# Kernel optimization log

Measured on AMD Instinct MI355X. Metric: run time of the kernel, lower is better.

## Reference

```python
import jax, jax.numpy as jnp
import numpy as np

B, D, H = 262144, 3, 64


def _mlp(params, x):
    # x: [D] -> scalar u
    (W1, b1), (W2, b2), (W3, b3), (W4, b4) = params
    h = jnp.tanh(x @ W1 + b1)
    h = jnp.tanh(h @ W2 + b2)
    h = jnp.tanh(h @ W3 + b3)
    return (h @ W4 + b4)[0]


def setup_inputs() -> dict:
    key = jax.random.key(0)
    ks = jax.random.split(key, 6)
    def glorot(k, shape):
        fan_in = shape[0]
        return jax.random.normal(k, shape, dtype=jnp.float32) / jnp.sqrt(jnp.float32(fan_in))
    return {
        "x_r": jax.random.normal(ks[0], (B, D), dtype=jnp.float32),
        "sigma_r": jax.random.uniform(ks[1], (B,), dtype=jnp.float32),
        "W1": glorot(ks[2], (D, H)), "b1": jnp.zeros((H,), jnp.float32),
        "W2": glorot(ks[3], (H, H)), "b2": jnp.zeros((H,), jnp.float32),
        "W3": glorot(ks[4], (H, H)), "b3": jnp.zeros((H,), jnp.float32),
        "W4": glorot(ks[5], (H, 1)), "b4": jnp.zeros((1,), jnp.float32),
    }


def reference(x_r, sigma_r, W1, b1, W2, b2, W3, b3, W4, b4):
    # r(x) = div( sigma * grad u(x) ) = trace( d(flux)/dx ), per sample.
    params = ((W1, b1), (W2, b2), (W3, b3), (W4, b4))

    def flux_single(x, s):
        # sigma * grad_u, shape [D]
        return s * jax.grad(lambda xx: _mlp(params, xx))(x)

    def div_single(x, s):
        # forward-over-reverse: jacfwd of reverse-mode grad -> [D, D]; take trace
        J = jax.jacfwd(lambda xx: flux_single(xx, s))(x)
        return jnp.trace(J)

    div = jax.vmap(div_single)(x_r, sigma_r)  # [B]
    return div[:, None]
```

## Files before the change

kernel.cpp:

```cpp
#include <hip/hip_runtime.h>

typedef __fp16 f16;
typedef f16  h8 __attribute__((ext_vector_type(8)));
typedef float f4 __attribute__((ext_vector_type(4)));
typedef unsigned u32t;

#define NBLOCKS 1024
#define WPB 4
#define SPW 64
#define NBATCH 4
#define XSTR 36
#define XST  (16 * XSTR)

union H8u { h8 v; u32t u[4]; };
union U4h { uint4 u; h8 v; };

__device__ __forceinline__ u32t pk2(float a, float b) {
    return __builtin_bit_cast(u32t, __builtin_amdgcn_cvt_pkrtz(a, b));
}

__device__ __forceinline__ void tanh_sech2(float a, float& h, float& g) {
    float E = __expf(2.f * a);
    float inv = __builtin_amdgcn_rcpf(E + 1.f);
    float u = inv + inv;
    h = 1.f - u;
    g = u * (2.f - u);
}

__global__ __launch_bounds__(256, 3) void pinn_mfma_kernel(
    const float* __restrict__ x_r, const float* __restrict__ sigma_r,
    const float* __restrict__ W1, const float* __restrict__ b1,
    const float* __restrict__ W2, const float* __restrict__ b2,
    const float* __restrict__ W3, const float* __restrict__ b3,
    const float* __restrict__ W4, float* __restrict__ out)
{
    __shared__ f4 Wg[64];
    __shared__ f4 Wb4[16], B2v[16], B3v[16], W4v[16];
    __shared__ u32t xch[WPB][5 * XST];

    const int tid = threadIdx.x, lane = tid & 63, wv = tid >> 6;
    const int sb = lane & 15;
    const int q  = lane >> 4;

    if (tid < 64) {
        float wx = W1[tid], wy = W1[64 + tid], wz = W1[128 + tid];
        f4 w; w[0] = wx; w[1] = wy; w[2] = wz;
        w[3] = -2.f * (wx * wx + wy * wy + wz * wz);
        Wg[tid] = w;
        ((float*)Wb4)[tid] = b1[tid];
        ((float*)B2v)[tid] = b2[tid];
        ((float*)B3v)[tid] = b3[tid];
        ((float*)W4v)[tid] = W4[tid];
    }
    __syncthreads();

    h8 A2f[4][2], A3f[4][2];
#pragma unroll
    for (int mt = 0; mt < 4; ++mt)
#pragma unroll
    for (int kk = 0; kk < 2; ++kk) {
        H8u t2, t3;
#pragma unroll
        for (int p = 0; p < 4; ++p) {
            const int r0 = (32 * kk + 8 * q + 2 * p) * 64 + 16 * mt + sb;
            t2.u[p] = pk2(W2[r0], W2[r0 + 64]);
            t3.u[p] = pk2(W3[r0], W3[r0 + 64]);
        }
        A2f[mt][kk] = t2.v; A3f[mt][kk] = t3.v;
    }

    u32t* xb = xch[wv];
    const int wbase = sb * XSTR + 2 * q;
    const int rbase = sb * XSTR + 4 * q;

    const long sbase = ((long)blockIdx.x * WPB + wv) * SPW;

    float nx0 = x_r[(sbase + sb) * 3], nx1 = x_r[(sbase + sb) * 3 + 1],
          nx2 = x_r[(sbase + sb) * 3 + 2], nsg = sigma_r[sbase + sb];

#define WR5(mt) { const int wo = wbase + 8 * (mt);                                         \
    *(uint2*)&xb[0 * XST + wo] = make_uint2(pk2(oh[0], oh[1]), pk2(oh[2], oh[3]));         \
    *(uint2*)&xb[1 * XST + wo] = make_uint2(pk2(ox[0], ox[1]), pk2(ox[2], ox[3]));         \
    *(uint2*)&xb[2 * XST + wo] = make_uint2(pk2(oy[0], oy[1]), pk2(oy[2], oy[3]));         \
    *(uint2*)&xb[3 * XST + wo] = make_uint2(pk2(oz[0], oz[1]), pk2(oz[2], oz[3]));         \
    *(uint2*)&xb[4 * XST + wo] = make_uint2(pk2(os[0], os[1]), pk2(os[2], os[3])); }

#define RDB(Bf, st) { U4h u0, u1;                                                          \
    u0.u = *(const uint4*)&xb[(st) * XST + rbase];                                         \
    u1.u = *(const uint4*)&xb[(st) * XST + rbase + 16];                                    \
    Bf[0] = u0.v; Bf[1] = u1.v; }

#define MFMA10(Af) _Pragma("unroll")                                                       \
    for (int kk = 0; kk < 2; ++kk) {                                                       \
        Ch = __builtin_amdgcn_mfma_f32_16x16x32_f16(Af[mt][kk], Bh[kk], Ch, 0, 0, 0);      \
        Cx = __builtin_amdgcn_mfma_f32_16x16x32_f16(Af[mt][kk], Bx[kk], Cx, 0, 0, 0);      \
        Cy = __builtin_amdgcn_mfma_f32_16x16x32_f16(Af[mt][kk], By[kk], Cy, 0, 0, 0);      \
        Cz = __builtin_amdgcn_mfma_f32_16x16x32_f16(Af[mt][kk], Bz[kk], Cz, 0, 0, 0);      \
        Cs = __builtin_amdgcn_mfma_f32_16x16x32_f16(Af[mt][kk], Bs[kk], Cs, 0, 0, 0);      \
    }

#pragma unroll 1
    for (int t = 0; t < NBATCH; ++t) {
        const float x0 = nx0, x1 = nx1, x2 = nx2, sg = nsg;
        const long sn = sbase + ((t + 1) & 3) * 16 + sb;
        nx0 = x_r[sn * 3]; nx1 = x_r[sn * 3 + 1]; nx2 = x_r[sn * 3 + 2];
        nsg = sigma_r[sn];

#pragma unroll
        for (int mt = 0; mt < 4; ++mt) {
            const f4 bb = Wb4[4 * mt + q];
            float oh[4], ox[4], oy[4], oz[4], os[4];
#pragma unroll
            for (int r = 0; r < 4; ++r) {
                const f4 w = Wg[16 * mt + 4 * q + r];
                float a = fmaf(w[0], x0, fmaf(w[1], x1, fmaf(w[2], x2, bb[r])));
                float h, g; tanh_sech2(a, h, g);
                oh[r] = h; ox[r] = g * w[0]; oy[r] = g * w[1]; oz[r] = g * w[2];
                os[r] = (h * g) * w[3];
            }
            WR5(mt)
        }

        h8 Bh[2], Bx[2], By[2], Bz[2], Bs[2];
        RDB(Bh, 0) RDB(Bx, 1) RDB(By, 2) RDB(Bz, 3) RDB(Bs, 4)

#pragma unroll
        for (int mt = 0; mt < 4; ++mt) {
            f4 Ch = {0.f,0.f,0.f,0.f}, Cx = {0.f,0.f,0.f,0.f}, Cy = {0.f,0.f,0.f,0.f},
               Cz = {0.f,0.f,0.f,0.f}, Cs = {0.f,0.f,0.f,0.f};
            MFMA10(A2f)
            const f4 bb = B2v[4 * mt + q];
            float oh[4], ox[4], oy[4], oz[4], os[4];
#pragma unroll
            for (int r = 0; r < 4; ++r) {
                float h, g; tanh_sech2(Ch[r] + bb[r], h, g);
                float ax = Cx[r], ay = Cy[r], az = Cz[r];
                float qq  = fmaf(ax, ax, fmaf(ay, ay, az * az));
                float hg2 = (h * g) * 2.f;
                oh[r] = h; ox[r] = g * ax; oy[r] = g * ay; oz[r] = g * az;
                os[r] = fmaf(g, Cs[r], -(hg2 * qq));
            }
            WR5(mt)
        }

        RDB(Bh, 0) RDB(Bx, 1) RDB(By, 2) RDB(Bz, 3) RDB(Bs, 4)

        float tot = 0.f;
#pragma unroll
        for (int mt = 0; mt < 4; ++mt) {
            f4 Ch = {0.f,0.f,0.f,0.f}, Cx = {0.f,0.f,0.f,0.f}, Cy = {0.f,0.f,0.f,0.f},
               Cz = {0.f,0.f,0.f,0.f}, Cs = {0.f,0.f,0.f,0.f};
            MFMA10(A3f)
            const f4 bb = B3v[4 * mt + q], w4 = W4v[4 * mt + q];
#pragma unroll
            for (int r = 0; r < 4; ++r) {
                float h, g; tanh_sech2(Ch[r] + bb[r], h, g);
                float ax = Cx[r], ay = Cy[r], az = Cz[r];
                float qq  = fmaf(ax, ax, fmaf(ay, ay, az * az));
                float hg2 = (h * g) * 2.f;
                float sv  = fmaf(g, Cs[r], -(hg2 * qq));
                tot = fmaf(sv, w4[r], tot);
            }
        }
        tot += __shfl_xor(tot, 16);
        tot += __shfl_xor(tot, 32);
        if (lane < 16) out[sbase + t * 16 + sb] = sg * tot;
    }
}

extern "C" void kernel_launch(void* const* d_in, const int* in_sizes, int n_in,
                              void* d_out, int out_size, void* d_ws, size_t ws_size,
                              hipStream_t stream) {
    const float* x_r     = (const float*)d_in[0];
    const float* sigma_r = (const float*)d_in[1];
    const float* W1      = (const float*)d_in[2];
    const float* b1      = (const float*)d_in[3];
    const float* W2      = (const float*)d_in[4];
    const float* b2      = (const float*)d_in[5];
    const float* W3      = (const float*)d_in[6];
    const float* b3      = (const float*)d_in[7];
    const float* W4      = (const float*)d_in[8];
    float* out = (float*)d_out;

    pinn_mfma_kernel<<<NBLOCKS, 256, 0, stream>>>(
        x_r, sigma_r, W1, b1, W2, b2, W3, b3, W4, out);
}
```

Measured before the change: 44.14 us.

## Use grid-stride batch loop with fewer blocks and fold 2/ln2 into tanh bias

Each wave no longer owns a fixed run of four 16-sample batches. Instead, 768 blocks walk batches with a grid-stride loop, and the next batch's x/sigma loads are prefetched. The tanh argument now goes straight to exp2, with the 2*log2(e) factor folded into precomputed biases and an FMA, which removes a multiply per activation. With fewer blocks, waves do an uneven number of batches, so load balance depends on how 768 blocks map onto the CUs.

```diff
diff --git a/kernel.cpp b/kernel.cpp
--- a/kernel.cpp
+++ b/kernel.cpp
@@ -5,12 +5,13 @@
 typedef float f4 __attribute__((ext_vector_type(4)));
 typedef unsigned u32t;
 
-#define NBLOCKS 1024
+#define NBLOCKS 768
 #define WPB 4
-#define SPW 64
-#define NBATCH 4
+#define NWAVES (NBLOCKS * WPB)
+#define NBAT (262144 / 16)
 #define XSTR 36
 #define XST  (16 * XSTR)
+#define K2L 2.8853900817779268f
 
 union H8u { h8 v; u32t u[4]; };
 union U4h { uint4 u; h8 v; };
@@ -19,8 +20,8 @@
     return __builtin_bit_cast(u32t, __builtin_amdgcn_cvt_pkrtz(a, b));
 }
 
-__device__ __forceinline__ void tanh_sech2(float a, float& h, float& g) {
-    float E = __expf(2.f * a);
+__device__ __forceinline__ void tanh_sech2_t(float t, float& h, float& g) {
+    float E = __builtin_amdgcn_exp2f(t);
     float inv = __builtin_amdgcn_rcpf(E + 1.f);
     float u = inv + inv;
     h = 1.f - u;
@@ -35,7 +36,7 @@
     const float* __restrict__ W4, float* __restrict__ out)
 {
     __shared__ f4 Wg[64];
-    __shared__ f4 Wb4[16], B2v[16], B3v[16], W4v[16];
+    __shared__ f4 Wb4[16], BbK2[16], BbK3[16], W4v[16];
     __shared__ u32t xch[WPB][5 * XST];
 
     const int tid = threadIdx.x, lane = tid & 63, wv = tid >> 6;
@@ -47,10 +48,10 @@
         f4 w; w[0] = wx; w[1] = wy; w[2] = wz;
         w[3] = -2.f * (wx * wx + wy * wy + wz * wz);
         Wg[tid] = w;
-        ((float*)Wb4)[tid] = b1[tid];
-        ((float*)B2v)[tid] = b2[tid];
-        ((float*)B3v)[tid] = b3[tid];
-        ((float*)W4v)[tid] = W4[tid];
+        ((float*)Wb4)[tid]  = b1[tid];
+        ((float*)BbK2)[tid] = K2L * b2[tid];
+        ((float*)BbK3)[tid] = K2L * b3[tid];
+        ((float*)W4v)[tid]  = W4[tid];
     }
     __syncthreads();
 
@@ -73,10 +74,7 @@
     const int wbase = sb * XSTR + 2 * q;
     const int rbase = sb * XSTR + 4 * q;
 
-    const long sbase = ((long)blockIdx.x * WPB + wv) * SPW;
-
-    float nx0 = x_r[(sbase + sb) * 3], nx1 = x_r[(sbase + sb) * 3 + 1],
-          nx2 = x_r[(sbase + sb) * 3 + 2], nsg = sigma_r[sbase + sb];
+    const int wave_global = blockIdx.x * WPB + wv;
 
 #define WR5(mt) { const int wo = wbase + 8 * (mt);                                         \
     *(uint2*)&xb[0 * XST + wo] = make_uint2(pk2(oh[0], oh[1]), pk2(oh[2], oh[3]));         \
@@ -99,10 +97,20 @@
         Cs = __builtin_amdgcn_mfma_f32_16x16x32_f16(Af[mt][kk], Bs[kk], Cs, 0, 0, 0);      \
     }
 
+    int b = wave_global;
+    {
+        const long sp = (long)b * 16 + sb;
+    }
+    long sp0 = (long)b * 16 + sb;
+    float nx0 = x_r[sp0 * 3], nx1 = x_r[sp0 * 3 + 1], nx2 = x_r[sp0 * 3 + 2],
+          nsg = sigma_r[sp0];
+
 #pragma unroll 1
-    for (int t = 0; t < NBATCH; ++t) {
+    for (; b < NBAT; b += NWAVES) {
         const float x0 = nx0, x1 = nx1, x2 = nx2, sg = nsg;
-        const long sn = sbase + ((t + 1) & 3) * 16 + sb;
+        int bn = b + NWAVES;
+        if (bn >= NBAT) bn = wave_global;
+        const long sn = (long)bn * 16 + sb;
         nx0 = x_r[sn * 3]; nx1 = x_r[sn * 3 + 1]; nx2 = x_r[sn * 3 + 2];
         nsg = sigma_r[sn];
 
@@ -113,8 +121,8 @@
 #pragma unroll
             for (int r = 0; r < 4; ++r) {
                 const f4 w = Wg[16 * mt + 4 * q + r];
-                float a = fmaf(w[0], x0, fmaf(w[1], x1, fmaf(w[2], x2, bb[r])));
-                float h, g; tanh_sech2(a, h, g);
+                const float a = fmaf(w[0], x0, fmaf(w[1], x1, fmaf(w[2], x2, bb[r])));
+                float h, g; tanh_sech2_t(K2L * a, h, g);
                 oh[r] = h; ox[r] = g * w[0]; oy[r] = g * w[1]; oz[r] = g * w[2];
                 os[r] = (h * g) * w[3];
             }
@@ -129,14 +137,14 @@
             f4 Ch = {0.f,0.f,0.f,0.f}, Cx = {0.f,0.f,0.f,0.f}, Cy = {0.f,0.f,0.f,0.f},
                Cz = {0.f,0.f,0.f,0.f}, Cs = {0.f,0.f,0.f,0.f};
             MFMA10(A2f)
-            const f4 bb = B2v[4 * mt + q];
+            const f4 bb = BbK2[4 * mt + q];
             float oh[4], ox[4], oy[4], oz[4], os[4];
 #pragma unroll
             for (int r = 0; r < 4; ++r) {
-                float h, g; tanh_sech2(Ch[r] + bb[r], h, g);
-                float ax = Cx[r], ay = Cy[r], az = Cz[r];
-                float qq  = fmaf(ax, ax, fmaf(ay, ay, az * az));
-                float hg2 = (h * g) * 2.f;
+                float h, g; tanh_sech2_t(fmaf(Ch[r], K2L, bb[r]), h, g);
+                const float ax = Cx[r], ay = Cy[r], az = Cz[r];
+                const float qq  = fmaf(ax, ax, fmaf(ay, ay, az * az));
+                const float hg2 = (h * g) * 2.f;
                 oh[r] = h; ox[r] = g * ax; oy[r] = g * ay; oz[r] = g * az;
                 os[r] = fmaf(g, Cs[r], -(hg2 * qq));
             }
@@ -151,20 +159,20 @@
             f4 Ch = {0.f,0.f,0.f,0.f}, Cx = {0.f,0.f,0.f,0.f}, Cy = {0.f,0.f,0.f,0.f},
                Cz = {0.f,0.f,0.f,0.f}, Cs = {0.f,0.f,0.f,0.f};
             MFMA10(A3f)
-            const f4 bb = B3v[4 * mt + q], w4 = W4v[4 * mt + q];
+            const f4 bb = BbK3[4 * mt + q], w4 = W4v[4 * mt + q];
 #pragma unroll
             for (int r = 0; r < 4; ++r) {
-                float h, g; tanh_sech2(Ch[r] + bb[r], h, g);
-                float ax = Cx[r], ay = Cy[r], az = Cz[r];
-                float qq  = fmaf(ax, ax, fmaf(ay, ay, az * az));
-                float hg2 = (h * g) * 2.f;
-                float sv  = fmaf(g, Cs[r], -(hg2 * qq));
+                float h, g; tanh_sech2_t(fmaf(Ch[r], K2L, bb[r]), h, g);
+                const float ax = Cx[r], ay = Cy[r], az = Cz[r];
+                const float qq  = fmaf(ax, ax, fmaf(ay, ay, az * az));
+                const float hg2 = (h * g) * 2.f;
+                const float sv  = fmaf(g, Cs[r], -(hg2 * qq));
                 tot = fmaf(sv, w4[r], tot);
             }
         }
         tot += __shfl_xor(tot, 16);
         tot += __shfl_xor(tot, 32);
-        if (lane < 16) out[sbase + t * 16 + sb] = sg * tot;
+        if (lane < 16) out[(long)b * 16 + sb] = sg * tot;
     }
 }
 
```

Result: faster. 42.64 us (-3.4%).
